# Kernel optimization log

Measured on AMD Instinct MI355X. Metric: run time of the kernel, lower is better.

## Reference

```python
import jax, jax.numpy as jnp
import numpy as np

SEQ_LEN, BATCH, INPUT_SIZE, HIDDEN = 512, 64, 256, 512


def setup_inputs() -> dict:
    key = jax.random.key(0)
    k_x, k_wih, k_whh, k_bih, k_bhh = jax.random.split(key, 5)
    bound = 1.0 / np.sqrt(HIDDEN)  # torch nn.RNN init: U(-1/sqrt(H), 1/sqrt(H))
    x = jax.random.normal(k_x, (SEQ_LEN, BATCH, INPUT_SIZE), dtype=jnp.float32)
    h0 = jnp.zeros((1, BATCH, HIDDEN), dtype=jnp.float32)
    W_ih = jax.random.uniform(k_wih, (HIDDEN, INPUT_SIZE), minval=-bound, maxval=bound, dtype=jnp.float32)
    W_hh = jax.random.uniform(k_whh, (HIDDEN, HIDDEN), minval=-bound, maxval=bound, dtype=jnp.float32)
    b_ih = jax.random.uniform(k_bih, (HIDDEN,), minval=-bound, maxval=bound, dtype=jnp.float32)
    b_hh = jax.random.uniform(k_bhh, (HIDDEN,), minval=-bound, maxval=bound, dtype=jnp.float32)
    return {"x": x, "h0": h0, "W_ih": W_ih, "W_hh": W_hh, "b_ih": b_ih, "b_hh": b_hh}


def reference(x, h0, W_ih, W_hh, b_ih, b_hh):
    # Elman RNN: h_t = tanh(W_ih x_t + b_ih + W_hh h_{t-1} + b_hh)
    # Precompute the input projection for all timesteps (one big GEMM),
    # then scan the sequential recurrence.
    xW = jnp.einsum('tbi,hi->tbh', x, W_ih) + b_ih + b_hh  # (T, B, H)

    def step(h, xw_t):
        h_new = jnp.tanh(xw_t + h @ W_hh.T)  # (B, H)
        return h_new, h_new

    h_last, h_seq = jax.lax.scan(step, h0[0], xW)
    return h_seq, h_last[None]  # (T, B, H), (1, B, H)
```

## Files before the change

### kernel.cpp

```cpp
#include <hip/hip_runtime.h>


#define T_LEN 512
#define NBATCH 64
#define ISZ 256
#define HSZ 512

typedef __attribute__((ext_vector_type(8))) short short8;
typedef __attribute__((ext_vector_type(4))) int int4v;
typedef __attribute__((ext_vector_type(4))) float f32x4;

__device__ __forceinline__ unsigned short f2bf(float f) {
  unsigned u = __float_as_uint(f);
  u += 0x7fffu + ((u >> 16) & 1u);
  return (unsigned short)(u >> 16);
}
__device__ __forceinline__ float bf2f(unsigned short h) {
  return __uint_as_float(((unsigned)h) << 16);
}

__device__ __forceinline__ void split_bf(f32x4 a, f32x4 b, short8& hi, short8& lo) {
#pragma unroll
  for (int i = 0; i < 4; ++i) {
    unsigned short h = f2bf(a[i]);
    hi[i] = (short)h;
    lo[i] = (short)f2bf(a[i] - bf2f(h));
    unsigned short h2 = f2bf(b[i]);
    hi[i + 4] = (short)h2;
    lo[i + 4] = (short)f2bf(b[i] - bf2f(h2));
  }
}

__device__ __forceinline__ float fast_tanh(float x) {
  float e = __expf(2.0f * x);
  return 1.0f - 2.0f * __builtin_amdgcn_rcpf(1.0f + e);
}

__global__ __launch_bounds__(512) void xw_proj(
    const float* __restrict__ x, const float* __restrict__ Wih,
    const float* __restrict__ bih, const float* __restrict__ bhh,
    float* __restrict__ out) {
  __shared__ __align__(16) short xhi[16][264];
  __shared__ __align__(16) short xlo[16][264];

  const int tid = threadIdx.x;
  const int w  = tid >> 6;
  const int L  = tid & 63;
  const int lr = L & 15;
  const int lg = L >> 4;

  const int mhalf = blockIdx.x & 1;
  const int grp   = blockIdx.x >> 1;

  short8 Ahi[2][8], Alo[2][8];
  f32x4 bias[2];
  int mt[2];
#pragma unroll
  for (int m = 0; m < 2; ++m) {
    mt[m] = mhalf * 16 + 2 * w + m;
    int j = mt[m] * 16 + lr;
#pragma unroll
    for (int kt = 0; kt < 8; ++kt) {
      int k = kt * 32 + lg * 8;
      const f32x4 v0 = *(const f32x4*)(Wih + j * ISZ + k);
      const f32x4 v1 = *(const f32x4*)(Wih + j * ISZ + k + 4);
      split_bf(v0, v1, Ahi[m][kt], Alo[m][kt]);
    }
    int j0 = mt[m] * 16 + lg * 4;
    f32x4 b1 = *(const f32x4*)(bih + j0);
    f32x4 b2 = *(const f32x4*)(bhh + j0);
    bias[m] = b1 + b2;
  }

  for (int it = 0; it < 8; ++it) {
    const int tau = grp * 8 + it;
    const int t = tau >> 2;
    const int g = tau & 3;

    __syncthreads();
    {
      const int f   = tid * 8;
      const int row = f >> 8;
      const int i0  = f & 255;
      const float* p = x + ((size_t)(t * NBATCH + g * 16 + row) * ISZ + i0);
      const f32x4 v0 = *(const f32x4*)p;
      const f32x4 v1 = *(const f32x4*)(p + 4);
      short8 hi, lo;
      split_bf(v0, v1, hi, lo);
      *(short8*)(&xhi[row][i0]) = hi;
      *(short8*)(&xlo[row][i0]) = lo;
    }
    __syncthreads();

    f32x4 acc[2];
    acc[0] = f32x4{0.f, 0.f, 0.f, 0.f};
    acc[1] = f32x4{0.f, 0.f, 0.f, 0.f};
#pragma unroll
    for (int kt = 0; kt < 8; ++kt) {
      int koff = kt * 32 + lg * 8;
      short8 bh = *(const short8*)(&xhi[lr][koff]);
      short8 bl = *(const short8*)(&xlo[lr][koff]);
      acc[0] = __builtin_amdgcn_mfma_f32_16x16x32_bf16(Ahi[0][kt], bh, acc[0], 0, 0, 0);
      acc[1] = __builtin_amdgcn_mfma_f32_16x16x32_bf16(Ahi[1][kt], bh, acc[1], 0, 0, 0);
      acc[0] = __builtin_amdgcn_mfma_f32_16x16x32_bf16(Alo[0][kt], bh, acc[0], 0, 0, 0);
      acc[1] = __builtin_amdgcn_mfma_f32_16x16x32_bf16(Alo[1][kt], bh, acc[1], 0, 0, 0);
      acc[0] = __builtin_amdgcn_mfma_f32_16x16x32_bf16(Ahi[0][kt], bl, acc[0], 0, 0, 0);
      acc[1] = __builtin_amdgcn_mfma_f32_16x16x32_bf16(Ahi[1][kt], bl, acc[1], 0, 0, 0);
    }
#pragma unroll
    for (int m = 0; m < 2; ++m) {
      f32x4 r = acc[m] + bias[m];
      *(f32x4*)(out + (size_t)((((t * 4 + g) * 32 + mt[m]) * 64) + L) * 4) = r;
    }
  }
}

__global__ __launch_bounds__(512, 2) void rnn_scan_i8w8(
    const float* __restrict__ Whh, const float* __restrict__ h0,
    float* __restrict__ out) {
  __shared__ __align__(16) char hb[2][16][528];

  const int tid = threadIdx.x;
  const int w  = tid >> 6;
  const int L  = tid & 63;
  const int lr = L & 15;
  const int lg = L >> 4;
  const int g  = blockIdx.x;

  const float QS  = 127.0f * 22.627416997969522f;
  const float DEQ = 1.0f / (127.0f * 127.0f * 22.627416997969522f);

  int4v A[4][8];
#pragma unroll
  for (int m = 0; m < 4; ++m) {
    const int j = (4 * w + m) * 16 + lr;
#pragma unroll
    for (int kt = 0; kt < 8; ++kt) {
      const float* p = Whh + (size_t)j * HSZ + kt * 64 + lg * 16;
      int dw[4];
#pragma unroll
      for (int d = 0; d < 4; ++d) {
        f32x4 v = *(const f32x4*)(p + d * 4);
        int pk = 0;
#pragma unroll
        for (int i = 0; i < 4; ++i) {
          float q = __builtin_rintf(fminf(fmaxf(v[i] * QS, -127.f), 127.f));
          pk |= ((int)q & 255) << (8 * i);
        }
        dw[d] = pk;
      }
      A[m][kt] = int4v{dw[0], dw[1], dw[2], dw[3]};
    }
  }

  {
    const int row = tid >> 5;
    const int k0  = (tid & 31) * 16;
    const float* p = h0 + ((size_t)(g * 16 + row) * HSZ + k0);
    int dw[4];
#pragma unroll
    for (int c = 0; c < 4; ++c) {
      f32x4 v = *(const f32x4*)(p + c * 4);
      int pk = 0;
#pragma unroll
      for (int i = 0; i < 4; ++i) {
        float q = __builtin_rintf(fminf(fmaxf(v[i] * 127.f, -127.f), 127.f));
        pk |= ((int)q & 255) << (8 * i);
      }
      dw[c] = pk;
    }
    *(int4v*)(&hb[0][row][k0]) = int4v{dw[0], dw[1], dw[2], dw[3]};
  }
  __syncthreads();

  int j0m[4];
#pragma unroll
  for (int m = 0; m < 4; ++m) j0m[m] = (4 * w + m) * 16 + lg * 4;

  f32x4 xwn[4];
#pragma unroll
  for (int m = 0; m < 4; ++m)
    xwn[m] = *(const f32x4*)(out + (size_t)((g * 32 + 4 * w + m) * 64 + L) * 4);

  f32x4 pend[4];

  auto step = [&](int t, int cur) {
    f32x4 xwc[4];
#pragma unroll
    for (int m = 0; m < 4; ++m) xwc[m] = xwn[m];

    const int tn = (t < T_LEN - 1) ? t + 1 : t;
#pragma unroll
    for (int m = 0; m < 4; ++m)
      xwn[m] = *(const f32x4*)(out + (size_t)(((tn * 4 + g) * 32 + 4 * w + m) * 64 + L) * 4);

    if (t > 0) {
#pragma unroll
      for (int m = 0; m < 4; ++m)
        *(f32x4*)(out + ((size_t)((t - 1) * NBATCH + g * 16 + lr) * HSZ + j0m[m])) = pend[m];
    }

    int4v acc[4];
#pragma unroll
    for (int m = 0; m < 4; ++m) acc[m] = int4v{0, 0, 0, 0};
#pragma unroll
    for (int kt = 0; kt < 8; ++kt) {
      int4v B = *(const int4v*)(&hb[cur][lr][kt * 64 + lg * 16]);
#pragma unroll
      for (int m = 0; m < 4; ++m)
        acc[m] = __builtin_amdgcn_mfma_i32_16x16x64_i8(A[m][kt], B, acc[m], 0, 0, 0);
    }

    const int nxt = cur ^ 1;
#pragma unroll
    for (int m = 0; m < 4; ++m) {
      f32x4 h;
      int q[4];
#pragma unroll
      for (int r = 0; r < 4; ++r) {
        float y = (float)acc[m][r] * DEQ + xwc[m][r];
        float hv = fast_tanh(y);
        h[r] = hv;
        q[r] = (int)__builtin_rintf(hv * 127.f);
      }
      pend[m] = h;
      unsigned d = (unsigned)(q[0] & 255) | ((unsigned)(q[1] & 255) << 8) |
                   ((unsigned)(q[2] & 255) << 16) | ((unsigned)q[3] << 24);
      *(unsigned*)(&hb[nxt][lr][j0m[m]]) = d;
    }
    __syncthreads();
  };

  for (int t = 0; t < T_LEN; t += 2) {
    step(t, 0);
    step(t + 1, 1);
  }

#pragma unroll
  for (int m = 0; m < 4; ++m) {
    *(f32x4*)(out + ((size_t)((T_LEN - 1) * NBATCH + g * 16 + lr) * HSZ + j0m[m])) = pend[m];
    *(f32x4*)(out + (size_t)T_LEN * NBATCH * HSZ +
              ((size_t)(g * 16 + lr) * HSZ + j0m[m])) = pend[m];
  }
}

extern "C" void kernel_launch(void* const* d_in, const int* in_sizes, int n_in,
                              void* d_out, int out_size, void* d_ws, size_t ws_size,
                              hipStream_t stream) {
  const float* x   = (const float*)d_in[0];
  const float* h0  = (const float*)d_in[1];
  const float* Wih = (const float*)d_in[2];
  const float* Whh = (const float*)d_in[3];
  const float* bih = (const float*)d_in[4];
  const float* bhh = (const float*)d_in[5];
  float* out = (float*)d_out;

  xw_proj<<<512, 512, 0, stream>>>(x, Wih, bih, bhh, out);
  rnn_scan_i8w8<<<4, 512, 0, stream>>>(Whh, h0, out);
}
```

Before: 1.026 ms.

## Fuse input projection and recurrence into one kernel with flag-based producer/consumer overlap

Merges the input projection GEMM and the sequential scan into a single launch. 252 producer blocks compute projections per (timestep, batch group) and publish completion through atomic flags, while 4 scan blocks spin on those flags so the recurrence can start before the whole projection finishes. The projection also drops the W_ih low-bf16 term (fewer MFMAs, lower precision), and the tanh and int8 packing in the scan use exp2, fma and perm tricks. In exchange it relies on all blocks being co-resident to avoid deadlock, and adds an extra init kernel plus atomic polling.

```diff
diff --git a/kernel.cpp b/kernel.cpp
--- a/kernel.cpp
+++ b/kernel.cpp
@@ -5,6 +5,7 @@
 #define NBATCH 64
 #define ISZ 256
 #define HSZ 512
+#define NPROJ 252
 
 typedef __attribute__((ext_vector_type(8))) short short8;
 typedef __attribute__((ext_vector_type(4))) int int4v;
@@ -19,29 +20,14 @@
   return __uint_as_float(((unsigned)h) << 16);
 }
 
-__device__ __forceinline__ void split_bf(f32x4 a, f32x4 b, short8& hi, short8& lo) {
-#pragma unroll
-  for (int i = 0; i < 4; ++i) {
-    unsigned short h = f2bf(a[i]);
-    hi[i] = (short)h;
-    lo[i] = (short)f2bf(a[i] - bf2f(h));
-    unsigned short h2 = f2bf(b[i]);
-    hi[i + 4] = (short)h2;
-    lo[i + 4] = (short)f2bf(b[i] - bf2f(h2));
-  }
-}
-
-__device__ __forceinline__ float fast_tanh(float x) {
-  float e = __expf(2.0f * x);
-  return 1.0f - 2.0f * __builtin_amdgcn_rcpf(1.0f + e);
-}
-
-__global__ __launch_bounds__(512) void xw_proj(
-    const float* __restrict__ x, const float* __restrict__ Wih,
+__global__ void init_flags(int* f) { f[blockIdx.x * 512 + threadIdx.x] = 0; }
+
+__global__ __launch_bounds__(512, 2) void rnn_fused(
+    const float* __restrict__ x, const float* __restrict__ h0,
+    const float* __restrict__ Wih, const float* __restrict__ Whh,
     const float* __restrict__ bih, const float* __restrict__ bhh,
-    float* __restrict__ out) {
-  __shared__ __align__(16) short xhi[16][264];
-  __shared__ __align__(16) short xlo[16][264];
+    float* __restrict__ out, int* __restrict__ flags) {
+  __shared__ __align__(16) char smem[16896];
 
   const int tid = threadIdx.x;
   const int w  = tid >> 6;
@@ -49,86 +35,93 @@
   const int lr = L & 15;
   const int lg = L >> 4;
 
-  const int mhalf = blockIdx.x & 1;
-  const int grp   = blockIdx.x >> 1;
-
-  short8 Ahi[2][8], Alo[2][8];
-  f32x4 bias[2];
-  int mt[2];
-#pragma unroll
-  for (int m = 0; m < 2; ++m) {
-    mt[m] = mhalf * 16 + 2 * w + m;
-    int j = mt[m] * 16 + lr;
-#pragma unroll
-    for (int kt = 0; kt < 8; ++kt) {
-      int k = kt * 32 + lg * 8;
-      const f32x4 v0 = *(const f32x4*)(Wih + j * ISZ + k);
-      const f32x4 v1 = *(const f32x4*)(Wih + j * ISZ + k + 4);
-      split_bf(v0, v1, Ahi[m][kt], Alo[m][kt]);
-    }
-    int j0 = mt[m] * 16 + lg * 4;
-    f32x4 b1 = *(const f32x4*)(bih + j0);
-    f32x4 b2 = *(const f32x4*)(bhh + j0);
-    bias[m] = b1 + b2;
-  }
-
-  for (int it = 0; it < 8; ++it) {
-    const int tau = grp * 8 + it;
-    const int t = tau >> 2;
-    const int g = tau & 3;
-
-    __syncthreads();
-    {
-      const int f   = tid * 8;
-      const int row = f >> 8;
-      const int i0  = f & 255;
-      const float* p = x + ((size_t)(t * NBATCH + g * 16 + row) * ISZ + i0);
-      const f32x4 v0 = *(const f32x4*)p;
-      const f32x4 v1 = *(const f32x4*)(p + 4);
-      short8 hi, lo;
-      split_bf(v0, v1, hi, lo);
-      *(short8*)(&xhi[row][i0]) = hi;
-      *(short8*)(&xlo[row][i0]) = lo;
-    }
-    __syncthreads();
-
-    f32x4 acc[2];
-    acc[0] = f32x4{0.f, 0.f, 0.f, 0.f};
-    acc[1] = f32x4{0.f, 0.f, 0.f, 0.f};
-#pragma unroll
-    for (int kt = 0; kt < 8; ++kt) {
-      int koff = kt * 32 + lg * 8;
-      short8 bh = *(const short8*)(&xhi[lr][koff]);
-      short8 bl = *(const short8*)(&xlo[lr][koff]);
-      acc[0] = __builtin_amdgcn_mfma_f32_16x16x32_bf16(Ahi[0][kt], bh, acc[0], 0, 0, 0);
-      acc[1] = __builtin_amdgcn_mfma_f32_16x16x32_bf16(Ahi[1][kt], bh, acc[1], 0, 0, 0);
-      acc[0] = __builtin_amdgcn_mfma_f32_16x16x32_bf16(Alo[0][kt], bh, acc[0], 0, 0, 0);
-      acc[1] = __builtin_amdgcn_mfma_f32_16x16x32_bf16(Alo[1][kt], bh, acc[1], 0, 0, 0);
-      acc[0] = __builtin_amdgcn_mfma_f32_16x16x32_bf16(Ahi[0][kt], bl, acc[0], 0, 0, 0);
-      acc[1] = __builtin_amdgcn_mfma_f32_16x16x32_bf16(Ahi[1][kt], bl, acc[1], 0, 0, 0);
-    }
-#pragma unroll
-    for (int m = 0; m < 2; ++m) {
-      f32x4 r = acc[m] + bias[m];
-      *(f32x4*)(out + (size_t)((((t * 4 + g) * 32 + mt[m]) * 64) + L) * 4) = r;
-    }
-  }
-}
-
-__global__ __launch_bounds__(512, 2) void rnn_scan_i8w8(
-    const float* __restrict__ Whh, const float* __restrict__ h0,
-    float* __restrict__ out) {
-  __shared__ __align__(16) char hb[2][16][528];
-
-  const int tid = threadIdx.x;
-  const int w  = tid >> 6;
-  const int L  = tid & 63;
-  const int lr = L & 15;
-  const int lg = L >> 4;
-  const int g  = blockIdx.x;
+  if (blockIdx.x >= 4) {
+    const int pb = blockIdx.x - 4;
+    short (*xhi)[264] = (short(*)[264])smem;
+    short (*xlo)[264] = (short(*)[264])(smem + 8448);
+
+    short8 Ah[4][8];
+    f32x4 bias[4];
+#pragma unroll
+    for (int m = 0; m < 4; ++m) {
+      const int mt = 4 * w + m;
+      const int j = mt * 16 + lr;
+#pragma unroll
+      for (int kt = 0; kt < 8; ++kt) {
+        const float* p = Wih + (size_t)j * ISZ + kt * 32 + lg * 8;
+        const f32x4 v0 = *(const f32x4*)p;
+        const f32x4 v1 = *(const f32x4*)(p + 4);
+        short8 a;
+#pragma unroll
+        for (int i = 0; i < 4; ++i) {
+          a[i]     = (short)f2bf(v0[i]);
+          a[i + 4] = (short)f2bf(v1[i]);
+        }
+        Ah[m][kt] = a;
+      }
+      f32x4 b1 = *(const f32x4*)(bih + mt * 16 + lg * 4);
+      f32x4 b2 = *(const f32x4*)(bhh + mt * 16 + lg * 4);
+      bias[m] = b1 + b2;
+    }
+
+    for (int tau = pb; tau < T_LEN * 4; tau += NPROJ) {
+      const int t = tau >> 2;
+      const int g = tau & 3;
+
+      __syncthreads();
+      {
+        const int f   = tid * 8;
+        const int row = f >> 8;
+        const int i0  = f & 255;
+        const float* p = x + ((size_t)(t * NBATCH + g * 16 + row) * ISZ + i0);
+        const f32x4 v0 = *(const f32x4*)p;
+        const f32x4 v1 = *(const f32x4*)(p + 4);
+        short8 hi, lo;
+#pragma unroll
+        for (int i = 0; i < 4; ++i) {
+          unsigned short h1 = f2bf(v0[i]);
+          hi[i] = (short)h1; lo[i] = (short)f2bf(v0[i] - bf2f(h1));
+          unsigned short h2 = f2bf(v1[i]);
+          hi[i + 4] = (short)h2; lo[i + 4] = (short)f2bf(v1[i] - bf2f(h2));
+        }
+        *(short8*)(&xhi[row][i0]) = hi;
+        *(short8*)(&xlo[row][i0]) = lo;
+      }
+      __syncthreads();
+
+      f32x4 acc[4];
+#pragma unroll
+      for (int m = 0; m < 4; ++m) acc[m] = f32x4{0.f, 0.f, 0.f, 0.f};
+#pragma unroll
+      for (int kt = 0; kt < 8; ++kt) {
+        const int koff = kt * 32 + lg * 8;
+        short8 bh = *(const short8*)(&xhi[lr][koff]);
+        short8 bl = *(const short8*)(&xlo[lr][koff]);
+#pragma unroll
+        for (int m = 0; m < 4; ++m) {
+          acc[m] = __builtin_amdgcn_mfma_f32_16x16x32_bf16(Ah[m][kt], bh, acc[m], 0, 0, 0);
+          acc[m] = __builtin_amdgcn_mfma_f32_16x16x32_bf16(Ah[m][kt], bl, acc[m], 0, 0, 0);
+        }
+      }
+#pragma unroll
+      for (int m = 0; m < 4; ++m) {
+        f32x4 r = acc[m] + bias[m];
+        *(f32x4*)(out + (size_t)((((t * 4 + g) * 32 + 4 * w + m) * 64) + L) * 4) = r;
+      }
+      __syncthreads();
+      if (tid == 0) {
+        __threadfence();
+        atomicAdd(&flags[tau], 1);
+      }
+    }
+    return;
+  }
+
+  const int g = blockIdx.x;
+  char* hb = smem;
 
   const float QS  = 127.0f * 22.627416997969522f;
-  const float DEQ = 1.0f / (127.0f * 127.0f * 22.627416997969522f);
+  const float DEQ = (float)(1.0 / (127.0 * 127.0 * 22.627416997969522));
 
   int4v A[4][8];
 #pragma unroll
@@ -169,35 +162,43 @@
       }
       dw[c] = pk;
     }
-    *(int4v*)(&hb[0][row][k0]) = int4v{dw[0], dw[1], dw[2], dw[3]};
+    *(int4v*)(hb + row * 528 + k0) = int4v{dw[0], dw[1], dw[2], dw[3]};
+  }
+
+  if (tid == 0) {
+    while (__hip_atomic_load(&flags[g], __ATOMIC_ACQUIRE, __HIP_MEMORY_SCOPE_AGENT) == 0)
+      __builtin_amdgcn_s_sleep(2);
   }
   __syncthreads();
 
-  int j0m[4];
-#pragma unroll
-  for (int m = 0; m < 4; ++m) j0m[m] = (4 * w + m) * 16 + lg * 4;
-
-  f32x4 xwn[4];
-#pragma unroll
-  for (int m = 0; m < 4; ++m)
-    xwn[m] = *(const f32x4*)(out + (size_t)((g * 32 + 4 * w + m) * 64 + L) * 4);
+  const int j0 = 4 * w * 16 + lg * 4;
+  const char* xwp = (const char*)out + ((size_t)(g * 32 + 4 * w) * 64 + L) * 16;
+  float* hsp = out + (size_t)(g * 16 + lr) * HSZ + j0;
+  const int ldsr = lr * 528 + lg * 16;
+  const int ldsw = lr * 528 + j0;
 
   f32x4 pend[4];
 
-  auto step = [&](int t, int cur) {
-    f32x4 xwc[4];
-#pragma unroll
-    for (int m = 0; m < 4; ++m) xwc[m] = xwn[m];
-
-    const int tn = (t < T_LEN - 1) ? t + 1 : t;
+  for (int t = 0; t < T_LEN; ++t) {
+    const int cur = t & 1, nxt = cur ^ 1;
+
+    f32x4 xw[4];
 #pragma unroll
     for (int m = 0; m < 4; ++m)
-      xwn[m] = *(const f32x4*)(out + (size_t)(((tn * 4 + g) * 32 + 4 * w + m) * 64 + L) * 4);
+#pragma unroll
+      for (int r = 0; r < 4; ++r)
+        xw[m][r] = __hip_atomic_load((const float*)(xwp + m * 1024 + r * 4),
+                                     __ATOMIC_RELAXED, __HIP_MEMORY_SCOPE_AGENT);
+
+    int tf = (t < T_LEN - 1) ? t + 1 : t;
+    int fv = 1;
+    if (tid == 0)
+      fv = __hip_atomic_load(&flags[tf * 4 + g], __ATOMIC_RELAXED, __HIP_MEMORY_SCOPE_AGENT);
 
     if (t > 0) {
 #pragma unroll
-      for (int m = 0; m < 4; ++m)
-        *(f32x4*)(out + ((size_t)((t - 1) * NBATCH + g * 16 + lr) * HSZ + j0m[m])) = pend[m];
+      for (int m = 0; m < 4; ++m) *(f32x4*)(hsp + m * 16) = pend[m];
+      hsp += NBATCH * HSZ;
     }
 
     int4v acc[4];
@@ -205,42 +206,45 @@
     for (int m = 0; m < 4; ++m) acc[m] = int4v{0, 0, 0, 0};
 #pragma unroll
     for (int kt = 0; kt < 8; ++kt) {
-      int4v B = *(const int4v*)(&hb[cur][lr][kt * 64 + lg * 16]);
+      int4v B = *(const int4v*)(hb + cur * 8448 + ldsr + kt * 64);
 #pragma unroll
       for (int m = 0; m < 4; ++m)
         acc[m] = __builtin_amdgcn_mfma_i32_16x16x64_i8(A[m][kt], B, acc[m], 0, 0, 0);
     }
 
-    const int nxt = cur ^ 1;
 #pragma unroll
     for (int m = 0; m < 4; ++m) {
+      unsigned qi[4];
       f32x4 h;
-      int q[4];
 #pragma unroll
       for (int r = 0; r < 4; ++r) {
-        float y = (float)acc[m][r] * DEQ + xwc[m][r];
-        float hv = fast_tanh(y);
+        float y  = fmaf((float)acc[m][r], DEQ, xw[m][r]);
+        float e  = __builtin_amdgcn_exp2f(y * 2.8853900817779268f);
+        float rc = __builtin_amdgcn_rcpf(1.0f + e);
+        float hv = fmaf(-2.0f, rc, 1.0f);
         h[r] = hv;
-        q[r] = (int)__builtin_rintf(hv * 127.f);
+        qi[r] = __float_as_uint(fmaf(hv, 127.0f, 12582912.0f));
       }
       pend[m] = h;
-      unsigned d = (unsigned)(q[0] & 255) | ((unsigned)(q[1] & 255) << 8) |
-                   ((unsigned)(q[2] & 255) << 16) | ((unsigned)q[3] << 24);
-      *(unsigned*)(&hb[nxt][lr][j0m[m]]) = d;
+      unsigned p0 = __builtin_amdgcn_perm(qi[1], qi[0], 0x0c0c0400u);
+      unsigned p1 = __builtin_amdgcn_perm(qi[3], qi[2], 0x04000c0cu);
+      *(unsigned*)(hb + nxt * 8448 + ldsw + m * 16) = p0 | p1;
+    }
+
+    if (tid == 0 && fv == 0) {
+      while (__hip_atomic_load(&flags[tf * 4 + g], __ATOMIC_ACQUIRE,
+                               __HIP_MEMORY_SCOPE_AGENT) == 0)
+        __builtin_amdgcn_s_sleep(2);
     }
     __syncthreads();
-  };
-
-  for (int t = 0; t < T_LEN; t += 2) {
-    step(t, 0);
-    step(t + 1, 1);
+    xwp += 131072;
   }
 
 #pragma unroll
   for (int m = 0; m < 4; ++m) {
-    *(f32x4*)(out + ((size_t)((T_LEN - 1) * NBATCH + g * 16 + lr) * HSZ + j0m[m])) = pend[m];
+    *(f32x4*)(hsp + m * 16) = pend[m];
     *(f32x4*)(out + (size_t)T_LEN * NBATCH * HSZ +
-              ((size_t)(g * 16 + lr) * HSZ + j0m[m])) = pend[m];
+              (size_t)(g * 16 + lr) * HSZ + j0 + m * 16) = pend[m];
   }
 }
 
@@ -254,7 +258,8 @@
   const float* bih = (const float*)d_in[4];
   const float* bhh = (const float*)d_in[5];
   float* out = (float*)d_out;
-
-  xw_proj<<<512, 512, 0, stream>>>(x, Wih, bih, bhh, out);
-  rnn_scan_i8w8<<<4, 512, 0, stream>>>(Whh, h0, out);
-}
+  int* flags = (int*)d_ws;
+
+  init_flags<<<4, 512, 0, stream>>>(flags);
+  rnn_fused<<<4 + NPROJ, 512, 0, stream>>>(x, h0, Wih, Whh, bih, bhh, out, flags);
+}
```

New measurement: 1.764 ms. 1.72x slower.
